# Kernel optimization log

Measured on AMD Instinct MI355X. Metric: run time of the kernel, lower is better.

Reference implementation:

```python
import jax, jax.numpy as jnp
import numpy as np

N = 16          # num_transforms
BS = 128        # batch_size
D = 4096        # encoder dim
C, H, W = 3, 64, 64
TEMP = 0.5      # hyperparams.temperature
LAM_H = 1.0     # hyperparams.h
EPS = 1e-8      # torch CosineSimilarity eps


def setup_inputs() -> dict:
    key = jax.random.key(0)
    k1, k2, k3 = jax.random.split(key, 3)
    return {
        "pic_set": jax.random.normal(k1, (N, BS, C, H, W), dtype=jnp.float32),
        "dec_pics": jax.random.normal(k2, (N, BS, C, H, W), dtype=jnp.float32),
        "h": jax.random.normal(k3, (N, BS, D), dtype=jnp.float32),
    }


def _pos_neg_indices(n, bs):
    # Static (numpy) index construction replicating the boolean masks.
    # Positives of row i: all j != i with j % bs == i % bs (sorted, row-major),
    # Negatives of row i: all j with j % bs != i % bs (sorted).
    k = n * bs
    i = np.arange(k)
    cols = (i % bs)[:, None] + np.arange(n)[None, :] * bs          # (K, N)
    pos_idx = cols[cols != i[:, None]].reshape(k, n - 1)            # (K, N-1)
    jj = np.arange(k)
    neg_mask = (jj[None, :] % bs) != (i[:, None] % bs)              # (K, K)
    neg_idx = np.broadcast_to(jj, (k, k))[neg_mask].reshape(k, k - n)  # (K, K-N)
    return jnp.asarray(pos_idx), jnp.asarray(neg_idx)


def _nt_xent(h):
    n, bs, d = h.shape
    k = n * bs
    s = h.reshape(k, d)
    # CosineSimilarity(dim=2) with eps clamp on norms
    nrm = jnp.maximum(jnp.linalg.norm(s, axis=1), EPS)
    sn = s / nrm[:, None]
    simmat = (sn @ sn.T) / TEMP                                     # (K, K)
    pos_idx, neg_idx = _pos_neg_indices(n, bs)
    pos = jnp.take_along_axis(simmat, pos_idx, axis=1)              # (K, N-1)
    neg = jnp.take_along_axis(simmat, neg_idx, axis=1)              # (K, K-N)
    # CrossEntropyLoss(reduction='sum') with label 0 on logits
    # [pos_{i,m}, neg_i] == sum of logsumexp - pos; logsumexp over concat
    # factors as logaddexp(lse(neg_i), pos_{i,m}).
    neg_lse = jax.scipy.special.logsumexp(neg, axis=1)              # (K,)
    loss = jnp.sum(jnp.logaddexp(neg_lse[:, None], pos) - pos)
    kpos = k * (n - 1)
    return loss / kpos


def reference(pic_set, dec_pics, h):
    n, bs = pic_set.shape[0], pic_set.shape[1]
    loss_h = _nt_xent(h)
    # dec_pics[(i+1) % N] cyclic offset, then flat MSE (mean reduction)
    offset = (np.arange(n) + 1) % n
    p = pic_set.reshape(n, bs, -1)
    dshift = dec_pics.reshape(n, bs, -1)[offset]
    loss_pairs = jnp.mean((p - dshift) ** 2)
    return loss_pairs + LAM_H * loss_h
```

## Files before the change

### kernel.cpp

```cpp
#include <hip/hip_runtime.h>
#include <hip/hip_bf16.h>
#include <math.h>

#define N_T   16
#define BSZ   128
#define DDIM  4096
#define KROWS (N_T * BSZ)
#define CHW   (3 * 64 * 64)
#define S_PIC (BSZ * CHW)
#define T_MSE (N_T * S_PIC)
#define KPOS  (KROWS * (N_T - 1))

typedef short  bf16x8 __attribute__((ext_vector_type(8)));
typedef float  f32x4  __attribute__((ext_vector_type(4)));

__device__ __forceinline__ float waveReduceSum(float v) {
    for (int off = 32; off > 0; off >>= 1) v += __shfl_down(v, off, 64);
    return v;
}
__device__ __forceinline__ float waveReduceMax(float v) {
    for (int off = 32; off > 0; off >>= 1) v = fmaxf(v, __shfl_down(v, off, 64));
    return v;
}
__device__ __forceinline__ float blockReduceSum(float v) {
    __shared__ float s[8];
    int lane = threadIdx.x & 63, wid = threadIdx.x >> 6;
    v = waveReduceSum(v);
    if (lane == 0) s[wid] = v;
    __syncthreads();
    int nw = (blockDim.x + 63) >> 6;
    v = (threadIdx.x < nw) ? s[threadIdx.x] : 0.0f;
    if (wid == 0) v = waveReduceSum(v);
    return v;
}
__device__ __forceinline__ float blockReduceMax(float v) {
    __shared__ float s[8];
    int lane = threadIdx.x & 63, wid = threadIdx.x >> 6;
    v = waveReduceMax(v);
    if (lane == 0) s[wid] = v;
    __syncthreads();
    int nw = (blockDim.x + 63) >> 6;
    v = (threadIdx.x < nw) ? s[threadIdx.x] : -INFINITY;
    if (wid == 0) v = waveReduceMax(v);
    return v;
}

__global__ __launch_bounds__(256) void mse_kernel(const float* __restrict__ pic,
                                                  const float* __restrict__ dec,
                                                  float* __restrict__ acc) {
    const int n = blockIdx.y;
    const size_t off = (size_t)n * S_PIC + (size_t)blockIdx.x * 8192 + threadIdx.x * 4;
    const size_t doff = (size_t)(((n + 1) & (N_T - 1)) - n) * S_PIC;
    const float* p = pic + off;
    const float* d = dec + off + doff;
    float s0 = 0.f, s1 = 0.f, s2 = 0.f, s3 = 0.f;
#pragma unroll
    for (int k = 0; k < 8; k++) {
        float4 a = *(const float4*)(p + k * 1024);
        float4 b = *(const float4*)(d + k * 1024);
        float dx = a.x - b.x, dy = a.y - b.y, dz = a.z - b.z, dw = a.w - b.w;
        s0 += dx * dx; s1 += dy * dy; s2 += dz * dz; s3 += dw * dw;
    }
    float sum = (s0 + s1) + (s2 + s3);
    sum = blockReduceSum(sum);
    if (threadIdx.x == 0) atomicAdd(acc, sum);
}

__global__ void norm_kernel(const float* __restrict__ h,
                            __hip_bfloat16* __restrict__ hb) {
    const int row = blockIdx.x;
    const float* r = h + (size_t)row * DDIM;
    float ss = 0.0f;
    for (int k = threadIdx.x * 8; k < DDIM; k += blockDim.x * 8) {
        float4 v0 = *(const float4*)(r + k);
        float4 v1 = *(const float4*)(r + k + 4);
        ss += v0.x * v0.x + v0.y * v0.y + v0.z * v0.z + v0.w * v0.w;
        ss += v1.x * v1.x + v1.y * v1.y + v1.z * v1.z + v1.w * v1.w;
    }
    ss = blockReduceSum(ss);
    __shared__ float scale_s;
    if (threadIdx.x == 0) scale_s = 1.0f / fmaxf(sqrtf(ss), 1e-8f);
    __syncthreads();
    const float sc = scale_s;
    __hip_bfloat16* ob = hb + (size_t)row * DDIM;
    for (int k = threadIdx.x * 8; k < DDIM; k += blockDim.x * 8) {
        float4 v0 = *(const float4*)(r + k);
        float4 v1 = *(const float4*)(r + k + 4);
        __hip_bfloat16 t[8];
        t[0] = __float2bfloat16(v0.x * sc); t[1] = __float2bfloat16(v0.y * sc);
        t[2] = __float2bfloat16(v0.z * sc); t[3] = __float2bfloat16(v0.w * sc);
        t[4] = __float2bfloat16(v1.x * sc); t[5] = __float2bfloat16(v1.y * sc);
        t[6] = __float2bfloat16(v1.z * sc); t[7] = __float2bfloat16(v1.w * sc);
        *(bf16x8*)(ob + k) = *(const bf16x8*)t;
    }
}

__global__ __launch_bounds__(256) void gemm_mfma(const ushort* __restrict__ X,
                                                 float* __restrict__ Cpart) {
    __shared__ ushort As[128 * 32];
    __shared__ ushort Bs[128 * 32];
    const int tid  = threadIdx.x;
    const int wave = tid >> 6, lane = tid & 63;
    const int wm = wave >> 1, wn = wave & 1;
    const int quad = lane >> 4, l16 = lane & 15;
    const int bi = blockIdx.y, bj = blockIdx.x;
    const int kz = blockIdx.z;

    f32x4 acc[4][4];
#pragma unroll
    for (int i = 0; i < 4; i++)
#pragma unroll
        for (int j = 0; j < 4; j++) acc[i][j] = (f32x4){0.f, 0.f, 0.f, 0.f};

    const int srow = lane >> 2;
    const int scol = (lane & 3) * 8;
    const ushort* Ag0 = X + (size_t)(bi * 128 + wave * 16       + srow) * DDIM + scol;
    const ushort* Ag1 = X + (size_t)(bi * 128 + (wave + 4) * 16 + srow) * DDIM + scol;
    const ushort* Bg0 = X + (size_t)(bj * 128 + wave * 16       + srow) * DDIM + scol;
    const ushort* Bg1 = X + (size_t)(bj * 128 + (wave + 4) * 16 + srow) * DDIM + scol;
    ushort* Al0 = As + wave * 512;
    ushort* Al1 = As + (wave + 4) * 512;
    ushort* Bl0 = Bs + wave * 512;
    ushort* Bl1 = Bs + (wave + 4) * 512;

    const int k0 = kz * (DDIM / 2), k1 = k0 + (DDIM / 2);
    for (int kk = k0; kk < k1; kk += 32) {
        __syncthreads();
        __builtin_amdgcn_global_load_lds(
            (const __attribute__((address_space(1))) unsigned int*)(Ag0 + kk),
            (__attribute__((address_space(3))) unsigned int*)Al0, 16, 0, 0);
        __builtin_amdgcn_global_load_lds(
            (const __attribute__((address_space(1))) unsigned int*)(Ag1 + kk),
            (__attribute__((address_space(3))) unsigned int*)Al1, 16, 0, 0);
        __builtin_amdgcn_global_load_lds(
            (const __attribute__((address_space(1))) unsigned int*)(Bg0 + kk),
            (__attribute__((address_space(3))) unsigned int*)Bl0, 16, 0, 0);
        __builtin_amdgcn_global_load_lds(
            (const __attribute__((address_space(1))) unsigned int*)(Bg1 + kk),
            (__attribute__((address_space(3))) unsigned int*)Bl1, 16, 0, 0);
        __syncthreads();

        bf16x8 a[4], b[4];
#pragma unroll
        for (int t = 0; t < 4; t++)
            a[t] = *(const bf16x8*)(As + (wm * 64 + t * 16 + l16) * 32 + quad * 8);
#pragma unroll
        for (int t = 0; t < 4; t++)
            b[t] = *(const bf16x8*)(Bs + (wn * 64 + t * 16 + l16) * 32 + quad * 8);
#pragma unroll
        for (int mt = 0; mt < 4; mt++)
#pragma unroll
            for (int nt = 0; nt < 4; nt++)
                acc[mt][nt] = __builtin_amdgcn_mfma_f32_16x16x32_bf16(
                    a[mt], b[nt], acc[mt][nt], 0, 0, 0);
    }

    float* Cp = Cpart + (size_t)kz * KROWS * KROWS;
#pragma unroll
    for (int mt = 0; mt < 4; mt++) {
#pragma unroll
        for (int r = 0; r < 4; r++) {
            const int row = bi * 128 + wm * 64 + mt * 16 + quad * 4 + r;
            float* o = Cp + (size_t)row * KROWS + bj * 128 + wn * 64 + l16;
#pragma unroll
            for (int nt = 0; nt < 4; nt++) o[nt * 16] = 2.0f * acc[mt][nt][r];
        }
    }
}

__global__ void lse_kernel(const float* __restrict__ Cpart, float* __restrict__ acc) {
    const int i = blockIdx.x;
    __shared__ float srow[KROWS];
    const float* r0 = Cpart + (size_t)i * KROWS;
    const float* r1 = r0 + (size_t)KROWS * KROWS;
    for (int j = threadIdx.x; j < KROWS; j += blockDim.x) srow[j] = r0[j] + r1[j];
    __syncthreads();

    const int ires = i & (BSZ - 1);
    float m = -INFINITY;
    for (int j = threadIdx.x; j < KROWS; j += blockDim.x)
        if ((j & (BSZ - 1)) != ires) m = fmaxf(m, srow[j]);
    m = blockReduceMax(m);
    __shared__ float mS;
    if (threadIdx.x == 0) mS = m;
    __syncthreads();
    m = mS;
    float se = 0.0f;
    for (int j = threadIdx.x; j < KROWS; j += blockDim.x)
        if ((j & (BSZ - 1)) != ires) se += expf(srow[j] - m);
    se = blockReduceSum(se);

    if (threadIdx.x == 0) {
        const float neg_lse = m + logf(se);
        float loss = 0.0f;
#pragma unroll
        for (int t = 0; t < N_T; t++) {
            const int j = ires + t * BSZ;
            if (j == i) continue;
            const float x = neg_lse - srow[j];
            loss += (x > 0.0f) ? (x + log1pf(expf(-x))) : log1pf(expf(x));
        }
        atomicAdd(acc + 1, loss);
    }
}

__global__ void finalize_kernel(const float* __restrict__ acc, float* __restrict__ out) {
    if (threadIdx.x == 0 && blockIdx.x == 0)
        out[0] = acc[0] / (float)T_MSE + acc[1] / (float)KPOS;
}

extern "C" void kernel_launch(void* const* d_in, const int* in_sizes, int n_in,
                              void* d_out, int out_size, void* d_ws, size_t ws_size,
                              hipStream_t stream) {
    const float* pic = (const float*)d_in[0];
    float* dec = (float*)d_in[1];
    const float* h = (const float*)d_in[2];
    float* out = (float*)d_out;

    float* acc = (float*)d_ws;
    const size_t hbuf_bytes   = (size_t)KROWS * DDIM * sizeof(__hip_bfloat16);
    const size_t simmat_bytes = (size_t)2 * KROWS * KROWS * sizeof(float);
    __hip_bfloat16* hbuf;
    float* simmat;
    if (ws_size >= 256 + hbuf_bytes + simmat_bytes) {
        hbuf   = (__hip_bfloat16*)((char*)d_ws + 256);
        simmat = (float*)((char*)d_ws + 256 + hbuf_bytes);
    } else {
        hbuf   = (__hip_bfloat16*)dec;
        simmat = (float*)((char*)dec + hbuf_bytes);
    }

    hipMemsetAsync(d_ws, 0, 256, stream);
    mse_kernel<<<dim3(192, N_T), 256, 0, stream>>>(pic, dec, acc);
    norm_kernel<<<KROWS, 256, 0, stream>>>(h, hbuf);
    dim3 ggrid(KROWS / 128, KROWS / 128, 2);
    gemm_mfma<<<ggrid, 256, 0, stream>>>((const ushort*)hbuf, simmat);
    lse_kernel<<<KROWS, 256, 0, stream>>>(simmat, acc);
    finalize_kernel<<<1, 64, 0, stream>>>(acc, out);
}
```

Before: 328.7 us.

## Fuse MSE reduction blocks into GEMM launch and vectorize LSE row load

```diff
diff --git a/kernel.cpp b/kernel.cpp
--- a/kernel.cpp
+++ b/kernel.cpp
@@ -11,6 +11,9 @@
 #define T_MSE (N_T * S_PIC)
 #define KPOS  (KROWS * (N_T - 1))
 
+#define GEMM_BLOCKS 512
+#define MSE_BLOCKS  3072
+
 typedef short  bf16x8 __attribute__((ext_vector_type(8)));
 typedef float  f32x4  __attribute__((ext_vector_type(4)));
 
@@ -45,14 +48,15 @@
     return v;
 }
 
-__global__ __launch_bounds__(256) void mse_kernel(const float* __restrict__ pic,
-                                                  const float* __restrict__ dec,
-                                                  float* __restrict__ acc) {
-    const int n = blockIdx.y;
-    const size_t off = (size_t)n * S_PIC + (size_t)blockIdx.x * 8192 + threadIdx.x * 4;
-    const size_t doff = (size_t)(((n + 1) & (N_T - 1)) - n) * S_PIC;
+__device__ __forceinline__ void mse_block(const float* __restrict__ pic,
+                                          const float* __restrict__ dec,
+                                          float* __restrict__ acc,
+                                          int n, int bx) {
+    const size_t off = (size_t)n * S_PIC + (size_t)bx * 8192 + threadIdx.x * 4;
+    const ptrdiff_t doff = (ptrdiff_t)(((n + 1) & (N_T - 1)) - n) * S_PIC;
     const float* p = pic + off;
-    const float* d = dec + off + doff;
+    const float* d = pic + off;
+    d = dec + off + doff;
     float s0 = 0.f, s1 = 0.f, s2 = 0.f, s3 = 0.f;
 #pragma unroll
     for (int k = 0; k < 8; k++) {
@@ -95,22 +99,33 @@
     }
 }
 
-__global__ __launch_bounds__(256) void gemm_mfma(const ushort* __restrict__ X,
-                                                 float* __restrict__ Cpart) {
+__global__ __launch_bounds__(256) void mega_kernel(const ushort* __restrict__ X,
+                                                   float* __restrict__ Cpart,
+                                                   const float* __restrict__ pic,
+                                                   const float* __restrict__ dec,
+                                                   float* __restrict__ acc) {
     __shared__ ushort As[128 * 32];
     __shared__ ushort Bs[128 * 32];
+    const int bid = blockIdx.x;
+
+    if (bid >= GEMM_BLOCKS) {
+        const int t = bid - GEMM_BLOCKS;
+        mse_block(pic, dec, acc, t & (N_T - 1), t >> 4);
+        return;
+    }
+
+    const int kz = bid >> 8;
+    const int bi = (bid >> 4) & 15, bj = bid & 15;
     const int tid  = threadIdx.x;
     const int wave = tid >> 6, lane = tid & 63;
     const int wm = wave >> 1, wn = wave & 1;
     const int quad = lane >> 4, l16 = lane & 15;
-    const int bi = blockIdx.y, bj = blockIdx.x;
-    const int kz = blockIdx.z;
-
-    f32x4 acc[4][4];
+
+    f32x4 acc_r[4][4];
 #pragma unroll
     for (int i = 0; i < 4; i++)
 #pragma unroll
-        for (int j = 0; j < 4; j++) acc[i][j] = (f32x4){0.f, 0.f, 0.f, 0.f};
+        for (int j = 0; j < 4; j++) acc_r[i][j] = (f32x4){0.f, 0.f, 0.f, 0.f};
 
     const int srow = lane >> 2;
     const int scol = (lane & 3) * 8;
@@ -151,8 +166,8 @@
         for (int mt = 0; mt < 4; mt++)
 #pragma unroll
             for (int nt = 0; nt < 4; nt++)
-                acc[mt][nt] = __builtin_amdgcn_mfma_f32_16x16x32_bf16(
-                    a[mt], b[nt], acc[mt][nt], 0, 0, 0);
+                acc_r[mt][nt] = __builtin_amdgcn_mfma_f32_16x16x32_bf16(
+                    a[mt], b[nt], acc_r[mt][nt], 0, 0, 0);
     }
 
     float* Cp = Cpart + (size_t)kz * KROWS * KROWS;
@@ -163,9 +178,15 @@
             const int row = bi * 128 + wm * 64 + mt * 16 + quad * 4 + r;
             float* o = Cp + (size_t)row * KROWS + bj * 128 + wn * 64 + l16;
 #pragma unroll
-            for (int nt = 0; nt < 4; nt++) o[nt * 16] = 2.0f * acc[mt][nt][r];
+            for (int nt = 0; nt < 4; nt++) o[nt * 16] = 2.0f * acc_r[mt][nt][r];
         }
     }
+}
+
+__global__ __launch_bounds__(256) void mse_kernel(const float* __restrict__ pic,
+                                                  const float* __restrict__ dec,
+                                                  float* __restrict__ acc) {
+    mse_block(pic, dec, acc, blockIdx.y, blockIdx.x);
 }
 
 __global__ void lse_kernel(const float* __restrict__ Cpart, float* __restrict__ acc) {
@@ -173,7 +194,12 @@
     __shared__ float srow[KROWS];
     const float* r0 = Cpart + (size_t)i * KROWS;
     const float* r1 = r0 + (size_t)KROWS * KROWS;
-    for (int j = threadIdx.x; j < KROWS; j += blockDim.x) srow[j] = r0[j] + r1[j];
+    for (int j = threadIdx.x * 4; j < KROWS; j += blockDim.x * 4) {
+        float4 a = *(const float4*)(r0 + j);
+        float4 b = *(const float4*)(r1 + j);
+        float4 s; s.x = a.x + b.x; s.y = a.y + b.y; s.z = a.z + b.z; s.w = a.w + b.w;
+        *(float4*)(srow + j) = s;
+    }
     __syncthreads();
 
     const int ires = i & (BSZ - 1);
@@ -220,21 +246,24 @@
     float* acc = (float*)d_ws;
     const size_t hbuf_bytes   = (size_t)KROWS * DDIM * sizeof(__hip_bfloat16);
     const size_t simmat_bytes = (size_t)2 * KROWS * KROWS * sizeof(float);
-    __hip_bfloat16* hbuf;
-    float* simmat;
+
+    hipMemsetAsync(d_ws, 0, 256, stream);
+
     if (ws_size >= 256 + hbuf_bytes + simmat_bytes) {
-        hbuf   = (__hip_bfloat16*)((char*)d_ws + 256);
-        simmat = (float*)((char*)d_ws + 256 + hbuf_bytes);
+        __hip_bfloat16* hbuf = (__hip_bfloat16*)((char*)d_ws + 256);
+        float* simmat = (float*)((char*)d_ws + 256 + hbuf_bytes);
+        norm_kernel<<<KROWS, 256, 0, stream>>>(h, hbuf);
+        mega_kernel<<<GEMM_BLOCKS + MSE_BLOCKS, 256, 0, stream>>>(
+            (const ushort*)hbuf, simmat, pic, dec, acc);
+        lse_kernel<<<KROWS, 256, 0, stream>>>(simmat, acc);
     } else {
-        hbuf   = (__hip_bfloat16*)dec;
-        simmat = (float*)((char*)dec + hbuf_bytes);
-    }
-
-    hipMemsetAsync(d_ws, 0, 256, stream);
-    mse_kernel<<<dim3(192, N_T), 256, 0, stream>>>(pic, dec, acc);
-    norm_kernel<<<KROWS, 256, 0, stream>>>(h, hbuf);
-    dim3 ggrid(KROWS / 128, KROWS / 128, 2);
-    gemm_mfma<<<ggrid, 256, 0, stream>>>((const ushort*)hbuf, simmat);
-    lse_kernel<<<KROWS, 256, 0, stream>>>(simmat, acc);
+        __hip_bfloat16* hbuf = (__hip_bfloat16*)dec;
+        float* simmat = (float*)((char*)dec + hbuf_bytes);
+        mse_kernel<<<dim3(MSE_BLOCKS / N_T, N_T), 256, 0, stream>>>(pic, dec, acc);
+        norm_kernel<<<KROWS, 256, 0, stream>>>(h, hbuf);
+        mega_kernel<<<GEMM_BLOCKS, 256, 0, stream>>>(
+            (const ushort*)hbuf, simmat, pic, dec, acc);
+        lse_kernel<<<KROWS, 256, 0, stream>>>(simmat, acc);
+    }
     finalize_kernel<<<1, 64, 0, stream>>>(acc, out);
 }
```

Result: faster. 305.0 us (-7.2%).
